# Performance work log

Measured on AMD Instinct MI355X. Metric: run time of the kernel, lower is better.

Reference implementation:

```python
import math
import jax, jax.numpy as jnp
import numpy as np


def _coeffs(alpha, delta, theta, gamma_real, gamma_imag):
    # alpha, delta: (D, N, 1); theta: (D, 1, 1); gamma_*: (D, N)
    D, N, _ = alpha.shape
    scale = math.sqrt(1.0 / float(N))
    th = jax.nn.sigmoid(theta.astype(jnp.float32)) * (2.0 * math.pi / float(N))  # (D,1,1)
    wavelets = jnp.arange(1, N + 1, dtype=jnp.float32).reshape(1, N, 1)
    phi = (wavelets * th)[:, :, 0]                      # (D, N) phase of q
    a = jax.nn.sigmoid(alpha.astype(jnp.float32))[:, :, 0]   # (D, N)
    d = jax.nn.sigmoid(delta.astype(jnp.float32))[:, :, 0]
    p = a                                               # (D, N)
    q_mag = 1.0 - a * d                                 # |q| in (0,1)
    gamma = (gamma_real.astype(jnp.float32) + 1j * gamma_imag.astype(jnp.float32)) * scale
    return p, q_mag, phi, gamma


def reference(x, alpha, delta, theta, gamma_real, gamma_imag, omega):
    # x: (B, D, L). FFT path (hx=None, compute_last_state=False).
    B, D, L = x.shape
    p, q_mag, phi, gamma = _coeffs(alpha, delta, theta, gamma_real, gamma_imag)
    gp = gamma * p.astype(jnp.complex64)                # (D, N) complex
    radius = jnp.minimum(q_mag, 1.0)                    # clamp(max=1.0)
    j = jnp.arange(L, dtype=jnp.float32)                # (L,)
    # q^j = radius^j * exp(i*phi*j); take real part of sum_n gp * q^j directly
    decay = jnp.exp(jnp.log(radius)[:, :, None] * j)    # (D, N, L)
    ang = phi[:, :, None] * j                           # (D, N, L)
    kernel_real = (jnp.einsum('dn,dnl->dl', jnp.real(gp), decay * jnp.cos(ang))
                   - jnp.einsum('dn,dnl->dl', jnp.imag(gp), decay * jnp.sin(ang)))  # (D, L)
    fft_len = 1 << int(2 * L - 1).bit_length()
    X = jnp.fft.rfft(x.astype(jnp.float32), n=fft_len, axis=-1)     # (B, D, F)
    K = jnp.fft.rfft(kernel_real, n=fft_len, axis=-1)               # (D, F)
    y = jnp.fft.irfft(X * K[None], n=fft_len, axis=-1)[..., :L]     # (B, D, L)
    residual = x * omega.astype(x.dtype)[None, :, None]
    return y.astype(x.dtype) + residual


def setup_inputs() -> dict:
    key = jax.random.key(0)
    B, D, L, N = 8, 1024, 2048, 16
    ks = jax.random.split(key, 7)
    x = jax.random.normal(ks[0], (B, D, L), dtype=jnp.float32)
    alpha = 0.2 * jax.random.normal(ks[1], (D, N, 1), dtype=jnp.float32)
    delta = 0.2 * jax.random.normal(ks[2], (D, N, 1), dtype=jnp.float32)
    # theta init: logit of permuted exponentially-spaced freqs (reset_parameters)
    rng = np.random.default_rng(0)
    freqs = np.exp(np.arange(1, D + 1, dtype=np.float32) * (-np.log(D) / D))
    freqs = rng.permutation(freqs)
    freqs = np.clip(freqs, 1e-6, 1.0 - 1e-6)
    theta = jnp.asarray(np.log(freqs / (1.0 - freqs)), dtype=jnp.float32).reshape(D, 1, 1)
    gamma_real = jax.random.normal(ks[3], (D, N), dtype=jnp.float32)
    gamma_imag = 0.1 * jax.random.normal(ks[4], (D, N), dtype=jnp.float32)
    omega = jnp.clip(0.25 * jax.random.normal(ks[5], (D,), dtype=jnp.float32), -1.0, 1.0)
    return {"x": x, "alpha": alpha, "delta": delta, "theta": theta,
            "gamma_real": gamma_real, "gamma_imag": gamma_imag, "omega": omega}
```

## Files before the change

### kernel.cpp

```cpp
#include <hip/hip_runtime.h>
#include <hip/hip_bf16.h>
#include <math.h>


#define Bc 8
#define Dc 1024
#define Lc 2048
#define FRAG_STRIDE 6144
#define SCANW_OFF (Dc * FRAG_STRIDE)
#define ECS 18

typedef _Float16 f16x8 __attribute__((ext_vector_type(8)));
typedef __fp16 h16x2 __attribute__((ext_vector_type(2)));
typedef float f32x4 __attribute__((ext_vector_type(4)));

__device__ inline uint pkh(float a, float b) {
    h16x2 p = __builtin_amdgcn_cvt_pkrtz(a, b);
    union { h16x2 v; uint u; } c; c.v = p;
    return c.u;
}

__device__ inline float2 upk(uint u) {
    union { uint v; __fp16 h[2]; } p; p.v = u;
    return make_float2((float)p.h[0], (float)p.h[1]);
}

__device__ inline f16x8 cvt8(float4 a, float4 b) {
    union { h16x2 h[4]; f16x8 v; } r;
    r.h[0] = __builtin_amdgcn_cvt_pkrtz(a.x, a.y);
    r.h[1] = __builtin_amdgcn_cvt_pkrtz(a.z, a.w);
    r.h[2] = __builtin_amdgcn_cvt_pkrtz(b.x, b.y);
    r.h[3] = __builtin_amdgcn_cvt_pkrtz(b.z, b.w);
    return r.v;
}

__global__ __launch_bounds__(512) void prep_kernel(const float* __restrict__ alpha,
        const float* __restrict__ delta, const float* __restrict__ theta,
        const float* __restrict__ gamma_r, const float* __restrict__ gamma_i,
        const float* __restrict__ omega, char* __restrict__ ws) {
    __shared__ float qpr[16 * 33];
    __shared__ float qpi[16 * 33];
    __shared__ float gprs[16], gpis[16], kap[33];
    const int tid = threadIdx.x;
    const int d = blockIdx.x;

    if (tid < 16) {
        int n = tid, idx = d * 16 + n;
        float a  = 1.f / (1.f + __expf(-alpha[idx]));
        float dl = 1.f / (1.f + __expf(-delta[idx]));
        float th = (1.f / (1.f + __expf(-theta[d]))) * (6.283185307179586f / 16.f);
        float phi = (float)(n + 1) * th;
        float radius = fminf(1.f - a * dl, 1.f);
        float sn, cs; __sincosf(phi, &sn, &cs);
        float qr_ = radius * cs, qi_ = radius * sn;
        gprs[n] = gamma_r[idx] * 0.25f * a;
        gpis[n] = gamma_i[idx] * 0.25f * a;
        float pr = 1.f, pi = 0.f;
        qpr[n * 33] = 1.f; qpi[n * 33] = 0.f;
        for (int j = 1; j <= 32; ++j) {
            float t2 = pr * qr_ - pi * qi_;
            pi = pr * qi_ + pi * qr_;
            pr = t2;
            qpr[n * 33 + j] = pr; qpi[n * 33 + j] = pi;
        }
    }
    __syncthreads();
    if (tid < 33) {
        float s = 0.f;
        #pragma unroll
        for (int n = 0; n < 16; ++n)
            s += gprs[n] * qpr[n * 33 + tid] - gpis[n] * qpi[n * 33 + tid];
        if (tid == 0) s += omega[d];
        kap[tid] = s;
    }
    __syncthreads();
    if (tid < 384) {
        int mat = tid >> 7;
        int sub = tid & 127;
        int rt = sub >> 6, ll = sub & 63;
        int row = rt * 16 + (ll & 15);
        int kb = 8 * (ll >> 4);
        union { _Float16 h[8]; f16x8 v; } fr;
        if (mat == 0) {
            #pragma unroll
            for (int j = 0; j < 8; ++j) {
                int dlt = row - (kb + j);
                fr.h[j] = (_Float16)((dlt >= 0) ? kap[dlt] : 0.f);
            }
        } else if (mat == 1) {
            #pragma unroll
            for (int j = 0; j < 8; ++j) {
                int k = kb + j, n = k >> 1;
                float qr_ = qpr[n * 33 + row + 1], qi_ = qpi[n * 33 + row + 1];
                float gr = gprs[n], gi = gpis[n];
                fr.h[j] = (_Float16)((k & 1) ? -(gr * qi_ + gi * qr_)
                                             : (gr * qr_ - gi * qi_));
            }
        } else {
            int n = row >> 1, im = row & 1;
            #pragma unroll
            for (int j = 0; j < 8; ++j) {
                int mm = kb + j;
                fr.h[j] = (_Float16)(im ? qpi[n * 33 + 31 - mm] : qpr[n * 33 + 31 - mm]);
            }
        }
        *(f16x8*)(ws + (size_t)d * FRAG_STRIDE + mat * 2048 + (rt * 64 + ll) * 16) = fr.v;
    } else if (tid < 400) {
        int n = tid - 384;
        float2* sw = (float2*)(ws + SCANW_OFF);
        sw[d * 16 + n] = make_float2(qpr[n * 33 + 32], qpi[n * 33 + 32]);
    }
}

__global__ __launch_bounds__(512) void ema_main(const float* __restrict__ x,
        const char* __restrict__ ws, float* __restrict__ out) {
    __shared__ uint ECall[8 * 64 * ECS];
    const int tid = threadIdx.x;
    const int w = tid >> 6;
    const int l = tid & 63;
    const int d = blockIdx.x;
    uint* EC = ECall + w * (64 * ECS);
    const int g = l >> 4;
    const int m = l & 15;
    const size_t rowoff = ((size_t)w * Dc + d) * Lc;
    const float4* xr4 = (const float4*)(x + rowoff);
    const f16x8* fr = (const f16x8*)(ws + (size_t)d * FRAG_STRIDE);

    f16x8 xf0, xf1, xf2, xf3;
    {
        const int base = m * 8 + 2 * g;
        float4 a0 = xr4[base],       b0 = xr4[base + 1];
        float4 a1 = xr4[base + 128], b1 = xr4[base + 129];
        float4 a2 = xr4[base + 256], b2 = xr4[base + 257];
        float4 a3 = xr4[base + 384], b3 = xr4[base + 385];
        xf0 = cvt8(a0, b0); xf1 = cvt8(a1, b1);
        xf2 = cvt8(a2, b2); xf3 = cvt8(a3, b3);
    }

    {
        f16x8 va0 = fr[256 + l], va1 = fr[320 + l];
        #define EMFMA(VA, RT, TC, XF) { \
            f32x4 acc = {0.f, 0.f, 0.f, 0.f}; \
            acc = __builtin_amdgcn_mfma_f32_16x16x32_f16(VA, XF, acc, 0, 0, 0); \
            uint2 u; u.x = pkh(acc[0], acc[1]); u.y = pkh(acc[2], acc[3]); \
            *(uint2*)&EC[(TC * 16 + m) * ECS + 8 * RT + 2 * g] = u; }
        EMFMA(va0, 0, 0, xf0) EMFMA(va0, 0, 1, xf1)
        EMFMA(va0, 0, 2, xf2) EMFMA(va0, 0, 3, xf3)
        EMFMA(va1, 1, 0, xf0) EMFMA(va1, 1, 1, xf1)
        EMFMA(va1, 1, 2, xf2) EMFMA(va1, 1, 3, xf3)
        #undef EMFMA
    }
    __syncthreads();

    float w1r[4], w1i[4], w2r[4], w2i[4], w3r[4], w3i[4];
    {
        const float2* sw = (const float2*)(ws + SCANW_OFF + (size_t)d * 128);
        #pragma unroll
        for (int j = 0; j < 4; ++j) {
            float2 t = sw[4 * g + j];
            w1r[j] = t.x; w1i[j] = t.y;
            w2r[j] = fmaf(w1r[j], w1r[j], -(w1i[j] * w1i[j]));
            w2i[j] = 2.f * w1r[j] * w1i[j];
            w3r[j] = fmaf(w2r[j], w1r[j], -(w2i[j] * w1i[j]));
            w3i[j] = fmaf(w2r[j], w1i[j],  (w2i[j] * w1r[j]));
        }
    }

    f16x8 ta0 = fr[l],       ta1 = fr[64 + l];
    f16x8 ga0 = fr[128 + l], ga1 = fr[192 + l];
    float4* or4 = (float4*)(out + rowoff);

    #pragma unroll
    for (int tc = 0; tc < 4; ++tc) {
        f16x8 xf = (tc == 0) ? xf0 : (tc == 1) ? xf1 : (tc == 2) ? xf2 : xf3;
        float cr_[4] = {0.f, 0.f, 0.f, 0.f};
        float ci_[4] = {0.f, 0.f, 0.f, 0.f};
        #pragma unroll
        for (int k = 1; k <= 4; ++k) {
            int c2 = tc * 16 + m - k;
            int cc = (c2 < 0) ? 0 : c2;
            uint2 e0 = *(const uint2*)&EC[cc * ECS + 4 * g];
            uint2 e1 = *(const uint2*)&EC[cc * ECS + 4 * g + 2];
            if (c2 >= 0) {
                float2 aa[4] = { upk(e0.x), upk(e0.y), upk(e1.x), upk(e1.y) };
                #pragma unroll
                for (int j = 0; j < 4; ++j) {
                    float wr_ = (k == 1) ? 1.f : (k == 2) ? w1r[j] :
                                (k == 3) ? w2r[j] : w3r[j];
                    float wi_ = (k == 1) ? 0.f : (k == 2) ? w1i[j] :
                                (k == 3) ? w2i[j] : w3i[j];
                    cr_[j] = fmaf(wr_, aa[j].x, fmaf(-wi_, aa[j].y, cr_[j]));
                    ci_[j] = fmaf(wr_, aa[j].y, fmaf( wi_, aa[j].x, ci_[j]));
                }
            }
        }
        union { h16x2 h[4]; f16x8 v; } cb;
        #pragma unroll
        for (int j = 0; j < 4; ++j)
            cb.h[j] = __builtin_amdgcn_cvt_pkrtz(cr_[j], ci_[j]);
        f32x4 y0 = {0.f, 0.f, 0.f, 0.f}, y1 = {0.f, 0.f, 0.f, 0.f};
        y0 = __builtin_amdgcn_mfma_f32_16x16x32_f16(ta0, xf,   y0, 0, 0, 0);
        y0 = __builtin_amdgcn_mfma_f32_16x16x32_f16(ga0, cb.v, y0, 0, 0, 0);
        y1 = __builtin_amdgcn_mfma_f32_16x16x32_f16(ta1, xf,   y1, 0, 0, 0);
        y1 = __builtin_amdgcn_mfma_f32_16x16x32_f16(ga1, cb.v, y1, 0, 0, 0);
        float4 o0, o1;
        o0.x = y0[0]; o0.y = y0[1]; o0.z = y0[2]; o0.w = y0[3];
        o1.x = y1[0]; o1.y = y1[1]; o1.z = y1[2]; o1.w = y1[3];
        or4[(tc * 16 + m) * 8 + g]     = o0;
        or4[(tc * 16 + m) * 8 + 4 + g] = o1;
    }
}

extern "C" void kernel_launch(void* const* d_in, const int* in_sizes, int n_in,
                              void* d_out, int out_size, void* d_ws, size_t ws_size,
                              hipStream_t stream) {
    const float* x       = (const float*)d_in[0];
    const float* alpha   = (const float*)d_in[1];
    const float* delta   = (const float*)d_in[2];
    const float* theta   = (const float*)d_in[3];
    const float* gamma_r = (const float*)d_in[4];
    const float* gamma_i = (const float*)d_in[5];
    const float* omega   = (const float*)d_in[6];
    float* out = (float*)d_out;
    char* ws = (char*)d_ws;

    prep_kernel<<<Dc, 512, 0, stream>>>(alpha, delta, theta,
                                        gamma_r, gamma_i, omega, ws);
    ema_main<<<Dc, 512, 0, stream>>>(x, ws, out);
}
```

Baseline: 35.23 us.

## Parallelize power table in prep, cut registers and move barrier in main

```diff
diff --git a/kernel.cpp b/kernel.cpp
--- a/kernel.cpp
+++ b/kernel.cpp
@@ -44,24 +44,23 @@
     const int tid = threadIdx.x;
     const int d = blockIdx.x;
 
-    if (tid < 16) {
-        int n = tid, idx = d * 16 + n;
+    {
+        int n = tid >> 5;
+        int j = (tid & 31) + 1;
+        int idx = d * 16 + n;
         float a  = 1.f / (1.f + __expf(-alpha[idx]));
         float dl = 1.f / (1.f + __expf(-delta[idx]));
         float th = (1.f / (1.f + __expf(-theta[d]))) * (6.283185307179586f / 16.f);
         float phi = (float)(n + 1) * th;
         float radius = fminf(1.f - a * dl, 1.f);
-        float sn, cs; __sincosf(phi, &sn, &cs);
-        float qr_ = radius * cs, qi_ = radius * sn;
-        gprs[n] = gamma_r[idx] * 0.25f * a;
-        gpis[n] = gamma_i[idx] * 0.25f * a;
-        float pr = 1.f, pi = 0.f;
-        qpr[n * 33] = 1.f; qpi[n * 33] = 0.f;
-        for (int j = 1; j <= 32; ++j) {
-            float t2 = pr * qr_ - pi * qi_;
-            pi = pr * qi_ + pi * qr_;
-            pr = t2;
-            qpr[n * 33 + j] = pr; qpi[n * 33 + j] = pi;
+        float rj = __expf((float)j * __logf(radius));
+        float sn, cs; __sincosf((float)j * phi, &sn, &cs);
+        qpr[n * 33 + j] = rj * cs;
+        qpi[n * 33 + j] = rj * sn;
+        if (j == 1) {
+            qpr[n * 33] = 1.f; qpi[n * 33] = 0.f;
+            gprs[n] = gamma_r[idx] * 0.25f * a;
+            gpis[n] = gamma_i[idx] * 0.25f * a;
         }
     }
     __syncthreads();
@@ -112,7 +111,7 @@
     }
 }
 
-__global__ __launch_bounds__(512) void ema_main(const float* __restrict__ x,
+__global__ __launch_bounds__(512, 8) void ema_main(const float* __restrict__ x,
         const char* __restrict__ ws, float* __restrict__ out) {
     __shared__ uint ECall[8 * 64 * ECS];
     const int tid = threadIdx.x;
@@ -150,24 +149,21 @@
         EMFMA(va1, 1, 2, xf2) EMFMA(va1, 1, 3, xf3)
         #undef EMFMA
     }
-    __syncthreads();
-
-    float w1r[4], w1i[4], w2r[4], w2i[4], w3r[4], w3i[4];
+
+    float w1r[4], w1i[4];
     {
         const float2* sw = (const float2*)(ws + SCANW_OFF + (size_t)d * 128);
         #pragma unroll
         for (int j = 0; j < 4; ++j) {
             float2 t = sw[4 * g + j];
             w1r[j] = t.x; w1i[j] = t.y;
-            w2r[j] = fmaf(w1r[j], w1r[j], -(w1i[j] * w1i[j]));
-            w2i[j] = 2.f * w1r[j] * w1i[j];
-            w3r[j] = fmaf(w2r[j], w1r[j], -(w2i[j] * w1i[j]));
-            w3i[j] = fmaf(w2r[j], w1i[j],  (w2i[j] * w1r[j]));
-        }
-    }
-
+        }
+    }
     f16x8 ta0 = fr[l],       ta1 = fr[64 + l];
     f16x8 ga0 = fr[128 + l], ga1 = fr[192 + l];
+
+    __syncthreads();
+
     float4* or4 = (float4*)(out + rowoff);
 
     #pragma unroll
@@ -175,6 +171,8 @@
         f16x8 xf = (tc == 0) ? xf0 : (tc == 1) ? xf1 : (tc == 2) ? xf2 : xf3;
         float cr_[4] = {0.f, 0.f, 0.f, 0.f};
         float ci_[4] = {0.f, 0.f, 0.f, 0.f};
+        float kr[4] = {1.f, 1.f, 1.f, 1.f};
+        float ki[4] = {0.f, 0.f, 0.f, 0.f};
         #pragma unroll
         for (int k = 1; k <= 4; ++k) {
             int c2 = tc * 16 + m - k;
@@ -185,12 +183,16 @@
                 float2 aa[4] = { upk(e0.x), upk(e0.y), upk(e1.x), upk(e1.y) };
                 #pragma unroll
                 for (int j = 0; j < 4; ++j) {
-                    float wr_ = (k == 1) ? 1.f : (k == 2) ? w1r[j] :
-                                (k == 3) ? w2r[j] : w3r[j];
-                    float wi_ = (k == 1) ? 0.f : (k == 2) ? w1i[j] :
-                                (k == 3) ? w2i[j] : w3i[j];
-                    cr_[j] = fmaf(wr_, aa[j].x, fmaf(-wi_, aa[j].y, cr_[j]));
-                    ci_[j] = fmaf(wr_, aa[j].y, fmaf( wi_, aa[j].x, ci_[j]));
+                    cr_[j] = fmaf(kr[j], aa[j].x, fmaf(-ki[j], aa[j].y, cr_[j]));
+                    ci_[j] = fmaf(kr[j], aa[j].y, fmaf( ki[j], aa[j].x, ci_[j]));
+                }
+            }
+            if (k < 4) {
+                #pragma unroll
+                for (int j = 0; j < 4; ++j) {
+                    float t2 = fmaf(kr[j], w1r[j], -(ki[j] * w1i[j]));
+                    ki[j] = fmaf(kr[j], w1i[j], ki[j] * w1r[j]);
+                    kr[j] = t2;
                 }
             }
         }
```

Result: slower. 51.24 us (+45.4%).
